# Kernel tuning notes

Measured on AMD Instinct MI355X. Metric: run time of the kernel, lower is better.

Reference implementation:

```python
import jax, jax.numpy as jnp
import numpy as np

S_D, I_D, O_D = 512, 256, 256
BATCH, T = 64, 1024
SNR = 10.0  # noise scale divisor, as in sample_stable_system
SPECTRAL_RADIUS = 0.95  # stable F, mirroring sample_stable_state_matrix


def setup_inputs() -> dict:
    key = jax.random.key(0)
    ks = jax.random.split(key, 9)
    A = np.asarray(jax.random.normal(ks[0], (S_D, S_D), dtype=jnp.float32))
    F = jnp.asarray(A * (SPECTRAL_RADIUS / np.linalg.norm(A, 2)))  # scale to spectral norm 0.95
    B_mat = jax.random.normal(ks[1], (S_D, I_D), dtype=jnp.float32)
    H = jax.random.normal(ks[2], (O_D, S_D), dtype=jnp.float32)
    sqrt_S_W = jax.random.normal(ks[3], (S_D, S_D), dtype=jnp.float32) / SNR
    sqrt_S_V = jax.random.normal(ks[4], (O_D, O_D), dtype=jnp.float32) / SNR
    state = jax.random.normal(ks[5], (BATCH, S_D), dtype=jnp.float32)
    inputs = jax.random.normal(ks[6], (BATCH, T, I_D), dtype=jnp.float32)
    W_noise = jax.random.normal(ks[7], (BATCH, T, S_D), dtype=jnp.float32)
    V_noise = jax.random.normal(ks[8], (BATCH, T, O_D), dtype=jnp.float32)
    return {"state": state, "inputs": inputs, "W_noise": W_noise, "V_noise": V_noise,
            "F": F, "B_mat": B_mat, "H": H, "sqrt_S_W": sqrt_S_W, "sqrt_S_V": sqrt_S_V}


def reference(state, inputs, W_noise, V_noise, F, B_mat, H, sqrt_S_W, sqrt_S_V):
    # Process noise W = eps_W @ sqrt_S_W.T, measurement noise V = eps_V @ sqrt_S_V.T
    W = jnp.einsum('bti,ji->btj', W_noise, sqrt_S_W)          # (B, T, S_D)
    V = jnp.einsum('bti,ji->btj', V_noise, sqrt_S_V)          # (B, T, O_D)
    drive = jnp.einsum('bti,ji->btj', inputs, B_mat) + W      # u_t @ B.T + W_t

    def step(s, u):  # s_t = s_{t-1} @ F.T + u_t
        s = s @ F.T + u
        return s, s

    _, states_t = jax.lax.scan(step, state, jnp.swapaxes(drive, 0, 1))  # (T, B, S_D)
    states = jnp.swapaxes(states_t, 0, 1)                                # (B, T, S_D)
    observations = jnp.einsum('bts,os->bto', states, H) + V              # (B, T, O_D)
    return states, observations
```

## Files before the change

### kernel.cpp

```cpp
#include <hip/hip_runtime.h>
#include <hip/hip_bf16.h>


typedef short bfrag __attribute__((ext_vector_type(8)));
typedef float f32x4 __attribute__((ext_vector_type(4)));

__device__ __host__ inline unsigned short f2bf(float f) {
    union { float f; unsigned u; } x; x.f = f;
    unsigned r = x.u + 0x7fffu + ((x.u >> 16) & 1u);
    return (unsigned short)(r >> 16);
}
__device__ inline float bf2f(unsigned short h) {
    union { unsigned u; float f; } x; x.u = ((unsigned)h) << 16;
    return x.f;
}

#define MSL 262144L

struct GemmDesc {
    const void* a0; const void* a1;
    const unsigned short* b;
    float* c;
    const unsigned short* cmbeta;
    unsigned short* cm;
    unsigned short* cmT;
    long a0_base, a0_os, a0_is;
    long a1_base, a1_os, a1_is;
    long a_zq, a_zr;
    long b_base, b_ldb, b_zq, b_zr;
    long c_base, c_os, c_is, c_zq, c_zr;
    long cm_base, cmb_base, cmT_base;
    long a_shift;
    int a0_icl, a1_icl, c_icl, zdivl;
    int ksplit, K, beta;
    int a0_f32, a1_f32;
    int gxl, gyl, gz_main;
    const unsigned short* xa; const unsigned short* xb;
    unsigned short* xcm; unsigned short* xcmT;
};

__global__ __launch_bounds__(256) void gemm_k(GemmDesc d) {
    __shared__ __align__(16) unsigned short As[2][128 * 64];
    __shared__ __align__(16) unsigned short Bs[2][128 * 64];
    const int tid  = threadIdx.x;
    const int lane = tid & 63;
    const int w    = tid >> 6;
    const int wrow = (w >> 1) * 64, wcol = (w & 1) * 64;

    const unsigned nx = gridDim.x, ny = gridDim.y;
    const unsigned nwg = nx * ny * gridDim.z;
    unsigned wid = blockIdx.x + nx * (blockIdx.y + ny * blockIdx.z);
    if ((nwg & 7) == 0) wid = (wid & 7) * (nwg >> 3) + (wid >> 3);
    const int bx = wid & (nx - 1);
    const int by = (wid >> d.gxl) & (ny - 1);
    int bz = wid >> (d.gxl + d.gyl);

    if (bz >= d.gz_main) {
        if (by >= 4) return;
        const long za = (long)(bz - d.gz_main) * MSL;
        d.a0 = d.xa; d.a0_base = za; d.a0_os = 512; d.a0_is = 0; d.a0_icl = 0;
        d.a0_f32 = 0; d.a1 = nullptr;
        d.b = d.xb; d.b_base = 0; d.b_ldb = 512; d.b_zq = d.b_zr = 0;
        d.K = 512; d.ksplit = 1 << 30; d.beta = 0; d.a_shift = 0;
        d.a_zq = d.a_zr = 0;
        d.c = nullptr; d.cm = d.xcm; d.cm_base = za;
        d.c_os = 512; d.c_is = 0; d.c_icl = 0; d.c_zq = d.c_zr = 0; d.c_base = 0;
        d.cmT = d.xcmT; d.cmT_base = za;
        bz = 0;
    }
    const long zq = (long)bz >> d.zdivl;
    const long zr = (long)bz & ((1L << d.zdivl) - 1);
    const int row0 = by * 128;
    const int col0 = bx * 128;

    const int g_r = tid >> 3;
    const int g_k = (tid & 7) * 8;
    const int swz = (g_r & 7) << 3;
    const long za_ = zq * d.a_zq + zr * d.a_zr;
    const long zb_ = zq * d.b_zq + zr * d.b_zr;

    const long m0a = (1L << d.a0_icl) - 1, m1a = (1L << d.a1_icl) - 1;
    long a0off[4], a1off[4], boff[4];
#pragma unroll
    for (int i = 0; i < 4; ++i) {
        long ar = (long)row0 + i * 32 + g_r - d.a_shift;
        if (ar < 0) ar = 0;
        a0off[i] = d.a0_base + za_ + (ar >> d.a0_icl) * d.a0_os + (ar & m0a) * d.a0_is;
        a1off[i] = d.a1 ? (d.a1_base + za_ + (ar >> d.a1_icl) * d.a1_os + (ar & m1a) * d.a1_is) : 0;
        boff[i]  = d.b_base + zb_ + (long)(col0 + i * 32 + g_r) * d.b_ldb;
    }

    bfrag ar_[4], br_[4];
    auto LOADT = [&](int t) {
        const int k0 = t * 64;
        const bool s1 = (k0 >= d.ksplit);
        const int kb = (s1 ? k0 - d.ksplit : k0) + g_k;
        if (s1 ? d.a1_f32 : d.a0_f32) {
            const float* fp = (const float*)(s1 ? d.a1 : d.a0);
#pragma unroll
            for (int i = 0; i < 4; ++i) {
                const float* p = fp + (s1 ? a1off[i] : a0off[i]) + kb;
                f32x4 x0 = *(const f32x4*)p, x1 = *(const f32x4*)(p + 4);
                union { bfrag v; unsigned short h[8]; } t_;
#pragma unroll
                for (int q = 0; q < 4; ++q) { t_.h[q] = f2bf(x0[q]); t_.h[4 + q] = f2bf(x1[q]); }
                ar_[i] = t_.v;
            }
        } else {
            const unsigned short* sp = (const unsigned short*)(s1 ? d.a1 : d.a0);
#pragma unroll
            for (int i = 0; i < 4; ++i)
                ar_[i] = *(const bfrag*)(sp + (s1 ? a1off[i] : a0off[i]) + kb);
        }
#pragma unroll
        for (int i = 0; i < 4; ++i) br_[i] = *(const bfrag*)(d.b + boff[i] + k0 + g_k);
    };
    auto WRT = [&](int buf) {
#pragma unroll
        for (int i = 0; i < 4; ++i) {
            *(bfrag*)&As[buf][(i * 32 + g_r) * 64 + (g_k ^ swz)] = ar_[i];
            *(bfrag*)&Bs[buf][(i * 32 + g_r) * 64 + (g_k ^ swz)] = br_[i];
        }
    };

    f32x4 acc[4][4] = {};
    const int nt = d.K / 64;

    LOADT(0); WRT(0); __syncthreads();
    int cur = 0;
    for (int t = 0; t < nt; ++t) {
        if (t + 1 < nt) LOADT(t + 1);
#pragma unroll
        for (int ks = 0; ks < 2; ++ks) {
            const int kk = ks * 32 + (lane >> 4) * 8;
            bfrag af[4], bf_[4];
#pragma unroll
            for (int mt = 0; mt < 4; ++mt) {
                const int r = wrow + mt * 16 + (lane & 15);
                af[mt] = *(const bfrag*)&As[cur][r * 64 + (kk ^ ((r & 7) << 3))];
            }
#pragma unroll
            for (int nn = 0; nn < 4; ++nn) {
                const int r = wcol + nn * 16 + (lane & 15);
                bf_[nn] = *(const bfrag*)&Bs[cur][r * 64 + (kk ^ ((r & 7) << 3))];
            }
#pragma unroll
            for (int mt = 0; mt < 4; ++mt)
#pragma unroll
                for (int nn = 0; nn < 4; ++nn)
                    acc[mt][nn] = __builtin_amdgcn_mfma_f32_16x16x32_bf16(
                        af[mt], bf_[nn], acc[mt][nn], 0, 0, 0);
        }
        if (t + 1 < nt) WRT(cur ^ 1);
        __syncthreads();
        cur ^= 1;
    }

    const long zc = zq * d.c_zq + zr * d.c_zr;
    const long mc = (1L << d.c_icl) - 1;
#pragma unroll
    for (int mt = 0; mt < 4; ++mt) {
        const int rb = row0 + wrow + mt * 16 + ((lane >> 4) << 2);
#pragma unroll
        for (int nn = 0; nn < 4; ++nn) {
            const int cc = col0 + wcol + nn * 16 + (lane & 15);
#pragma unroll
            for (int j = 0; j < 4; ++j) {
                const long r = rb + j;
                const long off = zc + (r >> d.c_icl) * d.c_os + (r & mc) * d.c_is + cc;
                float v = (r < d.a_shift) ? 0.0f : acc[mt][nn][j];
                if (d.beta == 2) v += bf2f(d.cmbeta[d.cmb_base + off]);
                if (d.c)  d.c[d.c_base + off] = v;
                if (d.cm) d.cm[d.cm_base + off] = f2bf(v);
                if (d.cmT) d.cmT[d.cmT_base + zc + (long)cc * 512 + r] = f2bf(v);
            }
        }
    }
}

__global__ void cvt_k(const float* src, unsigned short* dst, long n) {
    long i = ((long)blockIdx.x * 256 + threadIdx.x) * 8;
    const long stride = (long)gridDim.x * 256 * 8;
    for (; i < n; i += stride) {
        f32x4 x0 = *(const f32x4*)(src + i), x1 = *(const f32x4*)(src + i + 4);
        union { bfrag v; unsigned short h[8]; } t;
#pragma unroll
        for (int q = 0; q < 4; ++q) { t.h[q] = f2bf(x0[q]); t.h[4 + q] = f2bf(x1[q]); }
        *(bfrag*)(dst + i) = t.v;
    }
}

__global__ void build_ops_k(const float* F, const float* Bm, const float* H,
                            const float* sW, const float* sV,
                            unsigned short* bopd, unsigned short* bopo,
                            unsigned short* G1, unsigned short* Gt1) {
    int i = blockIdx.x * 256 + threadIdx.x;
    const int n1 = 512 * 768, n2 = 256 * 768, n3 = 512 * 512;
    if (i < n1) { int n = i / 768, k = i % 768;
        bopd[i] = f2bf(k < 256 ? Bm[n * 256 + k] : sW[n * 512 + (k - 256)]); return; }
    i -= n1;
    if (i < n2) { int o = i / 768, k = i % 768;
        bopo[i] = f2bf(k < 512 ? H[o * 512 + k] : sV[o * 256 + (k - 512)]); return; }
    i -= n2;
    if (i < n3) { G1[i] = f2bf(F[i]); return; }
    i -= n3;
    if (i < n3) { int r = i / 512, c = i % 512; Gt1[i] = f2bf(F[c * 512 + r]); }
}

__global__ void init_carry_k(const float* st0, const unsigned short* Smir,
                             unsigned short* dst) {
    const long i8 = ((long)blockIdx.x * 256 + threadIdx.x) * 8;
    if (i8 >= 4194304L) return;
    const long c = i8 >> 15, rem = i8 & 32767L;
    const long b = rem >> 9, s = rem & 511L;
    union { bfrag v; unsigned short h[8]; } t;
    if (c == 0) {
        const float* p = st0 + b * 512 + s;
        f32x4 x0 = *(const f32x4*)p, x1 = *(const f32x4*)(p + 4);
#pragma unroll
        for (int q = 0; q < 4; ++q) { t.h[q] = f2bf(x0[q]); t.h[4 + q] = f2bf(x1[q]); }
    } else {
        t.v = *(const bfrag*)(Smir + b * 524288L + (c - 1) * 4096L + 3584L + s);
    }
    *(bfrag*)(dst + i8) = t.v;
}

static GemmDesc D0() {
    GemmDesc d = {};
    d.zdivl = 30;
    d.ksplit = 1 << 30;
    d.b_ldb = 512; d.K = 512;
    d.gz_main = 1 << 30;
    return d;
}

extern "C" void kernel_launch(void* const* d_in, const int* in_sizes, int n_in,
                              void* d_out, int out_size, void* d_ws, size_t ws_size,
                              hipStream_t stream) {
    const float* st0 = (const float*)d_in[0];
    const float* inp = (const float*)d_in[1];
    const float* Wn  = (const float*)d_in[2];
    const float* Vn  = (const float*)d_in[3];
    const float* F   = (const float*)d_in[4];
    const float* Bm  = (const float*)d_in[5];
    const float* H   = (const float*)d_in[6];
    const float* sW  = (const float*)d_in[7];
    const float* sV  = (const float*)d_in[8];

    float* states = (float*)d_out;
    float* obs    = states + 33554432L;

    const long MS = MSL;
    const long CB = 32768;
    const int  NC = 128;
    const int  CL = 8;
    const long TOS = 524288;
    const long COS = (long)CL * 512;

    unsigned short* inpb = (unsigned short*)states;
    unsigned short* Wnb  = inpb + 16777216L;

    unsigned short* Smir = (unsigned short*)d_ws;
    unsigned short* G    = Smir + 33554432L;
    unsigned short* Gt   = G + 8 * MS;
    unsigned short* Qb   = Gt + 8 * MS;
    unsigned short* Qtb  = Qb + 6 * MS;
    unsigned short* BopD = Qtb + 6 * MS;
    unsigned short* BopO = BopD + 512 * 768;
    unsigned short* a0m  = BopO + 256 * 768;
    unsigned short* a1m  = a0m + (long)NC * CB;
    unsigned short* Vnb  = a1m + (long)NC * CB;
    (void)in_sizes; (void)n_in; (void)out_size; (void)ws_size;

    auto L = [&](const GemmDesc& d, int gx, int gxl, int gy, int gyl, int gz) {
        GemmDesc dd = d; dd.gxl = gxl; dd.gyl = gyl;
        gemm_k<<<dim3(gx, gy, gz), dim3(256), 0, stream>>>(dd);
    };

    cvt_k<<<dim3(2048), dim3(256), 0, stream>>>(inp, inpb, 16777216L);
    cvt_k<<<dim3(2048), dim3(256), 0, stream>>>(Wn, Wnb, 33554432L);
    cvt_k<<<dim3(2048), dim3(256), 0, stream>>>(Vn, Vnb, 16777216L);

    build_ops_k<<<dim3(4352), dim3(256), 0, stream>>>(F, Bm, H, sW, sV, BopD, BopO, G, Gt);

    {
        GemmDesc d = D0();
        d.a0 = inpb; d.a0_os = 256;
        d.a1 = Wnb;  d.a1_os = 512;
        d.ksplit = 256; d.K = 768;
        d.b = BopD; d.b_ldb = 768;
        d.cm = Smir; d.c_os = 512;
        L(d, 4, 2, 512, 9, 1);
    }

    for (int k = 1; k < CL; ++k) {
        GemmDesc d = D0();
        d.a0 = Smir; d.a0_base = (long)(k - 1) * 512;
        d.a0_icl = 7; d.a0_is = COS; d.a0_os = TOS;
        d.b = G;
        d.c_base = (long)k * 512;
        d.c_icl = 7; d.c_is = COS; d.c_os = TOS;
        d.beta = 2; d.cmbeta = Smir; d.cmb_base = (long)k * 512;
        d.cm = Smir; d.cm_base = (long)k * 512;
        d.gz_main = 1;
        int n;
        if (k == 1)      { d.xa = G;           d.xb = Gt;           d.xcm = G + MS;      d.xcmT = Gt + MS;      n = 1; }
        else if (k == 2) { d.xa = G;           d.xb = Gt + MS;      d.xcm = G + 2 * MS;  d.xcmT = Gt + 2 * MS;  n = 2; }
        else if (k == 3) { d.xa = G;           d.xb = Gt + 3 * MS;  d.xcm = G + 4 * MS;  d.xcmT = Gt + 4 * MS;  n = 4; }
        else if (k == 4) { d.xa = G + 7 * MS;  d.xb = Gt + 7 * MS;  d.xcm = Qb;          d.xcmT = Qtb;          n = 1; }
        else             { int j = k - 5;
                           d.xa = Qb + j * MS; d.xb = Qtb + j * MS; d.xcm = Qb + (j+1)*MS; d.xcmT = Qtb + (j+1)*MS; n = 1; }
        L(d, 4, 2, 64, 6, 1 + n);
    }

    init_carry_k<<<dim3(2048), dim3(256), 0, stream>>>(st0, Smir, a0m);

    unsigned short* curm = a0m;
    unsigned short* nxtm = a1m;
    for (int s = 1; s < NC; s <<= 1) {
        GemmDesc d = D0();
        d.a0 = curm; d.a0_os = 512;
        d.a_shift = (long)s * 64;
        if (s == 1) { d.b = G;  d.b_base = 7 * MS; }
        else        { d.b = Qb; d.b_base = (long)(__builtin_ctz(s) - 1) * MS; }
        d.beta = 2; d.cmbeta = curm; d.cmb_base = 0;
        d.cm = nxtm; d.c_os = 512;
        int n = 0;
        if (s == 1) { d.gz_main = 1; d.xa = Qb + 3 * MS; d.xb = Qtb + 3 * MS;
                      d.xcm = Qb + 4 * MS; d.xcmT = Qtb + 4 * MS; n = 1; }
        if (s == 2) { d.gz_main = 1; d.xa = Qb + 4 * MS; d.xb = Qtb + 4 * MS;
                      d.xcm = Qb + 5 * MS; d.xcmT = nullptr; n = 1; }
        L(d, 4, 2, 64, 6, 1 + n);
        unsigned short* tm = curm; curm = nxtm; nxtm = tm;
    }

    {
        GemmDesc d = D0();
        d.a0 = curm; d.a0_icl = 6; d.a0_os = CB; d.a0_is = 512;
        d.b = G; d.b_zr = MS;
        d.c = states; d.c_icl = 6; d.c_os = COS; d.c_is = TOS; d.c_zr = 512;
        d.beta = 2; d.cmbeta = Smir; d.cmb_base = 0;
        d.cm = Smir; d.cm_base = 0;
        L(d, 4, 2, 64, 6, 8);
    }

    {
        GemmDesc d = D0();
        d.a0 = Smir; d.a0_os = 512;
        d.a1 = Vnb;  d.a1_os = 256;
        d.ksplit = 512; d.K = 768;
        d.b = BopO; d.b_ldb = 768;
        d.c = obs; d.c_os = 256;
        L(d, 2, 1, 512, 9, 1);
    }
}
```

Baseline: 766.5 us.

## Fuse carry-correction and observation GEMMs into one kernel, convert V noise inline

Replaces the final carry-correction GEMM (states = carry@G^k + Smir) and the separate observation GEMM with one kernel. It keeps each 128-row block of corrected states in LDS as bf16 and immediately multiplies it by BopO. V noise is converted from fp32 to bf16 while loading instead of in a separate cvt pass. This removes a kernel launch, the bf16 states write-back and re-read, and the Vn conversion pass. In exchange it needs 160KB of LDS per 512-thread block, which gives low occupancy, and the grid has only 512 blocks.

```diff
diff --git a/kernel.cpp b/kernel.cpp
--- a/kernel.cpp
+++ b/kernel.cpp
@@ -178,6 +178,156 @@
     }
 }
 
+__global__ __launch_bounds__(512) void p3obs_k(
+        const unsigned short* __restrict__ carry, const unsigned short* __restrict__ Gm,
+        const unsigned short* __restrict__ Smir, const unsigned short* __restrict__ BopO,
+        const float* __restrict__ Vn, float* __restrict__ states, float* __restrict__ obs) {
+    __shared__ __align__(16) unsigned char lds[163840];
+    unsigned short* As1 = (unsigned short*)(lds);
+    unsigned short* Bs1 = (unsigned short*)(lds + 16384);
+    unsigned short* Sb  = (unsigned short*)(lds);
+    unsigned short* A2  = (unsigned short*)(lds);
+    unsigned short* Ts  = (unsigned short*)(lds + 131072);
+
+    const int tid  = threadIdx.x;
+    const int lane = tid & 63;
+    const int w    = tid >> 6;
+    const int wm   = w >> 2, wn = w & 3;
+    const int by   = blockIdx.y;
+    const int k    = blockIdx.z;
+    const unsigned short* G = Gm + (long)k * MSL;
+
+    f32x4 acc[4][8] = {};
+
+    for (int kt = 0; kt < 8; ++kt) {
+        __syncthreads();
+#pragma unroll
+        for (int i = 0; i < 2; ++i) {
+            const int fi = tid + i * 512;
+            const int row = fi >> 3, kk = (fi & 7) * 8;
+            const long rg = (long)by * 128 + row;
+            const long c = rg >> 6, b = rg & 63;
+            bfrag v = *(const bfrag*)(carry + c * 32768 + b * 512 + kt * 64 + kk);
+            *(bfrag*)&As1[row * 64 + (kk ^ ((row & 7) << 3))] = v;
+        }
+#pragma unroll
+        for (int i = 0; i < 8; ++i) {
+            const int fi = tid + i * 512;
+            const int row = fi >> 3, kk = (fi & 7) * 8;
+            bfrag v = *(const bfrag*)(G + (long)row * 512 + kt * 64 + kk);
+            *(bfrag*)&Bs1[row * 64 + (kk ^ ((row & 7) << 3))] = v;
+        }
+        __syncthreads();
+#pragma unroll
+        for (int ks = 0; ks < 2; ++ks) {
+            const int kk = ks * 32 + (lane >> 4) * 8;
+            bfrag af[4], bf_[8];
+#pragma unroll
+            for (int mt = 0; mt < 4; ++mt) {
+                const int r = wm * 64 + mt * 16 + (lane & 15);
+                af[mt] = *(const bfrag*)&As1[r * 64 + (kk ^ ((r & 7) << 3))];
+            }
+#pragma unroll
+            for (int nt = 0; nt < 8; ++nt) {
+                const int n = wn * 128 + nt * 16 + (lane & 15);
+                bf_[nt] = *(const bfrag*)&Bs1[n * 64 + (kk ^ ((n & 7) << 3))];
+            }
+#pragma unroll
+            for (int mt = 0; mt < 4; ++mt)
+#pragma unroll
+                for (int nt = 0; nt < 8; ++nt)
+                    acc[mt][nt] = __builtin_amdgcn_mfma_f32_16x16x32_bf16(
+                        af[mt], bf_[nt], acc[mt][nt], 0, 0, 0);
+        }
+    }
+    __syncthreads();
+
+#pragma unroll
+    for (int mt = 0; mt < 4; ++mt) {
+#pragma unroll
+        for (int nt = 0; nt < 8; ++nt) {
+#pragma unroll
+            for (int j = 0; j < 4; ++j) {
+                const int lr = wm * 64 + mt * 16 + ((lane >> 4) << 2) + j;
+                const int cc = wn * 128 + nt * 16 + (lane & 15);
+                const long rg = (long)by * 128 + lr;
+                const long c = rg >> 6, b = rg & 63;
+                const long t = c * 8 + k;
+                float v = acc[mt][nt][j] + bf2f(Smir[b * 524288L + t * 512 + cc]);
+                states[b * 524288L + t * 512 + cc] = v;
+                Sb[lr * 512 + (cc ^ ((lr & 7) << 3))] = f2bf(v);
+            }
+        }
+    }
+
+    f32x4 acc2[4][4] = {};
+    for (int kt = 0; kt < 12; ++kt) {
+        __syncthreads();
+#pragma unroll
+        for (int i = 0; i < 4; ++i) {
+            const int fi = tid + i * 512;
+            const int row = fi >> 3, kk = (fi & 7) * 8;
+            bfrag v = *(const bfrag*)(BopO + (long)row * 768 + kt * 64 + kk);
+            *(bfrag*)&Ts[row * 64 + (kk ^ ((row & 7) << 3))] = v;
+        }
+        if (kt >= 8) {
+#pragma unroll
+            for (int i = 0; i < 2; ++i) {
+                const int fi = tid + i * 512;
+                const int row = fi >> 3, kk = (fi & 7) * 8;
+                const long rg = (long)by * 128 + row;
+                const long c = rg >> 6, b = rg & 63;
+                const long t = c * 8 + k;
+                const float* p = Vn + b * 262144L + t * 256 + (kt - 8) * 64 + kk;
+                f32x4 x0 = *(const f32x4*)p, x1 = *(const f32x4*)(p + 4);
+                union { bfrag v; unsigned short h[8]; } u;
+#pragma unroll
+                for (int q = 0; q < 4; ++q) { u.h[q] = f2bf(x0[q]); u.h[4 + q] = f2bf(x1[q]); }
+                *(bfrag*)&A2[row * 64 + (kk ^ ((row & 7) << 3))] = u.v;
+            }
+        }
+        __syncthreads();
+#pragma unroll
+        for (int ks = 0; ks < 2; ++ks) {
+            const int kk = ks * 32 + (lane >> 4) * 8;
+            bfrag af[4], bf_[4];
+#pragma unroll
+            for (int mt = 0; mt < 4; ++mt) {
+                const int r = wm * 64 + mt * 16 + (lane & 15);
+                af[mt] = (kt < 8)
+                    ? *(const bfrag*)&Sb[r * 512 + ((kt * 64 + kk) ^ ((r & 7) << 3))]
+                    : *(const bfrag*)&A2[r * 64 + (kk ^ ((r & 7) << 3))];
+            }
+#pragma unroll
+            for (int nt = 0; nt < 4; ++nt) {
+                const int n = wn * 64 + nt * 16 + (lane & 15);
+                bf_[nt] = *(const bfrag*)&Ts[n * 64 + (kk ^ ((n & 7) << 3))];
+            }
+#pragma unroll
+            for (int mt = 0; mt < 4; ++mt)
+#pragma unroll
+                for (int nt = 0; nt < 4; ++nt)
+                    acc2[mt][nt] = __builtin_amdgcn_mfma_f32_16x16x32_bf16(
+                        af[mt], bf_[nt], acc2[mt][nt], 0, 0, 0);
+        }
+    }
+#pragma unroll
+    for (int mt = 0; mt < 4; ++mt) {
+#pragma unroll
+        for (int nt = 0; nt < 4; ++nt) {
+#pragma unroll
+            for (int j = 0; j < 4; ++j) {
+                const int lr = wm * 64 + mt * 16 + ((lane >> 4) << 2) + j;
+                const int cc = wn * 64 + nt * 16 + (lane & 15);
+                const long rg = (long)by * 128 + lr;
+                const long c = rg >> 6, b = rg & 63;
+                const long t = c * 8 + k;
+                obs[b * 262144L + t * 256 + cc] = acc2[mt][nt][j];
+            }
+        }
+    }
+}
+
 __global__ void cvt_k(const float* src, unsigned short* dst, long n) {
     long i = ((long)blockIdx.x * 256 + threadIdx.x) * 8;
     const long stride = (long)gridDim.x * 256 * 8;
@@ -269,7 +419,6 @@
     unsigned short* BopO = BopD + 512 * 768;
     unsigned short* a0m  = BopO + 256 * 768;
     unsigned short* a1m  = a0m + (long)NC * CB;
-    unsigned short* Vnb  = a1m + (long)NC * CB;
     (void)in_sizes; (void)n_in; (void)out_size; (void)ws_size;
 
     auto L = [&](const GemmDesc& d, int gx, int gxl, int gy, int gyl, int gz) {
@@ -279,7 +428,6 @@
 
     cvt_k<<<dim3(2048), dim3(256), 0, stream>>>(inp, inpb, 16777216L);
     cvt_k<<<dim3(2048), dim3(256), 0, stream>>>(Wn, Wnb, 33554432L);
-    cvt_k<<<dim3(2048), dim3(256), 0, stream>>>(Vn, Vnb, 16777216L);
 
     build_ops_k<<<dim3(4352), dim3(256), 0, stream>>>(F, Bm, H, sW, sV, BopD, BopO, G, Gt);
 
@@ -334,23 +482,6 @@
         unsigned short* tm = curm; curm = nxtm; nxtm = tm;
     }
 
-    {
-        GemmDesc d = D0();
-        d.a0 = curm; d.a0_icl = 6; d.a0_os = CB; d.a0_is = 512;
-        d.b = G; d.b_zr = MS;
-        d.c = states; d.c_icl = 6; d.c_os = COS; d.c_is = TOS; d.c_zr = 512;
-        d.beta = 2; d.cmbeta = Smir; d.cmb_base = 0;
-        d.cm = Smir; d.cm_base = 0;
-        L(d, 4, 2, 64, 6, 8);
-    }
-
-    {
-        GemmDesc d = D0();
-        d.a0 = Smir; d.a0_os = 512;
-        d.a1 = Vnb;  d.a1_os = 256;
-        d.ksplit = 512; d.K = 768;
-        d.b = BopO; d.b_ldb = 768;
-        d.c = obs; d.c_os = 256;
-        L(d, 2, 1, 512, 9, 1);
-    }
-}
+    p3obs_k<<<dim3(1, 64, 8), dim3(512), 0, stream>>>(
+        curm, G, Smir, BopO, Vn, states, obs);
+}
```

Result: faster. 703.7 us (-8.2%).
